# Kernel optimization log

Hardware: AMD Instinct MI355X
Metric: run time of the kernel (lower is better)

## Reference

```python
import jax, jax.numpy as jnp
import numpy as np

N_NODES = 10000
N_EDGES = 640000
D_FEAT = 128


def setup_inputs() -> dict:
    key = jax.random.key(0)
    k1, k2, k3, k4 = jax.random.split(key, 4)
    edge_feat = jax.random.normal(k1, (N_EDGES, D_FEAT), dtype=jnp.float32)
    node_feat = jax.random.normal(k2, (N_NODES, D_FEAT), dtype=jnp.float32)
    recv_idx = jax.random.randint(k3, (N_EDGES,), 0, N_NODES, dtype=jnp.int64 if jax.config.jax_enable_x64 else jnp.int32)
    W = jax.random.normal(k4, (2 * D_FEAT, D_FEAT), dtype=jnp.float32) * (1.0 / np.sqrt(2 * D_FEAT))
    b = jnp.zeros((D_FEAT,), dtype=jnp.float32)
    return {"edge_feat": edge_feat, "node_feat": node_feat, "recv_idx": recv_idx, "W": W, "b": b}


def reference(edge_feat, node_feat, recv_idx, W, b):
    # Unsorted segment sum: scatter-add edge features into receiver nodes. [E,d] -> [N,d]
    n_nodes = node_feat.shape[0]
    agg = jax.ops.segment_sum(edge_feat, recv_idx, num_segments=n_nodes)
    # Concat node features with aggregated received-edge features. [N, 2d]
    collected = jnp.concatenate([node_feat, agg], axis=-1)
    # node_model: Linear(2d -> d)
    return collected @ W + b
```

## Files before the change

### kernel.cpp

```cpp
#include <hip/hip_runtime.h>

#define N_NODES 10000
#define N_EDGES 640000
#define D_FEAT 128

#define HB   64
#define HBLK 1024
#define EPB  (N_EDGES / HB)
#define BCS  10016

#define WS_BCNT   0
#define WS_BSUM   641024
#define WS_START  641088
#define WS_SORTED 651392
#define WS_AGG    1291392

__global__ __launch_bounds__(HBLK) void hist_kernel(
        const int* __restrict__ recv, int* __restrict__ bcnt) {
    __shared__ int h[N_NODES];
    for (int i = threadIdx.x; i < N_NODES; i += HBLK) h[i] = 0;
    __syncthreads();
    const int4* r4 = (const int4*)(recv + blockIdx.x * EPB);
    for (int i = threadIdx.x; i < EPB / 4; i += HBLK) {
        const int4 r = r4[i];
        atomicAdd(&h[r.x], 1);
        atomicAdd(&h[r.y], 1);
        atomicAdd(&h[r.z], 1);
        atomicAdd(&h[r.w], 1);
    }
    __syncthreads();
    int* dst = bcnt + blockIdx.x * BCS;
    for (int i = threadIdx.x; i < N_NODES; i += HBLK) dst[i] = h[i];
}

__global__ __launch_bounds__(256) void scan1_kernel(
        int* __restrict__ bcnt, int* __restrict__ start, int* __restrict__ bsum) {
    __shared__ int s_w[4];
    const int tid = threadIdx.x;
    const int n   = blockIdx.x * 256 + tid;
    const bool ok = (n < N_NODES);

    int tot = 0;
    if (ok) {
        int run = 0;
        #pragma unroll
        for (int b = 0; b < HB; ++b) {
            int* p = bcnt + b * BCS + n;
            const int c = *p;
            *p = run;
            run += c;
        }
        tot = run;
    }
    const int lane = tid & 63;
    const int wave = tid >> 6;
    int x = tot;
    #pragma unroll
    for (int off = 1; off < 64; off <<= 1) {
        int t = __shfl_up(x, off, 64);
        if (lane >= off) x += t;
    }
    if (lane == 63) s_w[wave] = x;
    __syncthreads();
    int woff = 0;
    #pragma unroll
    for (int k = 0; k < 3; ++k) woff += (k < wave) ? s_w[k] : 0;
    if (ok) start[n] = woff + x - tot;
    if (tid == 0) bsum[blockIdx.x] = s_w[0] + s_w[1] + s_w[2] + s_w[3];
}

__global__ __launch_bounds__(256) void scan2_kernel(
        const int* __restrict__ bsum, int* __restrict__ start) {
    __shared__ int s_boff;
    const int tid = threadIdx.x;
    if (tid == 0) {
        int acc = 0;
        for (int k = 0; k < (int)blockIdx.x; ++k) acc += bsum[k];
        s_boff = acc;
        if (blockIdx.x == 0) start[N_NODES] = N_EDGES;
    }
    __syncthreads();
    const int n = blockIdx.x * 256 + tid;
    if (n < N_NODES) start[n] += s_boff;
}

__global__ __launch_bounds__(HBLK) void reorder_kernel(
        const int* __restrict__ recv, const int* __restrict__ bcnt,
        const int* __restrict__ start, int* __restrict__ sorted) {
    __shared__ int cur[N_NODES];
    const int* rel = bcnt + blockIdx.x * BCS;
    for (int i = threadIdx.x; i < N_NODES; i += HBLK)
        cur[i] = start[i] + rel[i];
    __syncthreads();
    const int ebase = blockIdx.x * EPB;
    const int4* r4 = (const int4*)(recv + ebase);
    for (int i = threadIdx.x; i < EPB / 4; i += HBLK) {
        const int4 r = r4[i];
        const int e = ebase + i * 4;
        sorted[atomicAdd(&cur[r.x], 1)] = e + 0;
        sorted[atomicAdd(&cur[r.y], 1)] = e + 1;
        sorted[atomicAdd(&cur[r.z], 1)] = e + 2;
        sorted[atomicAdd(&cur[r.w], 1)] = e + 3;
    }
}

#define GW 16
__global__ __launch_bounds__(512) void gather_kernel(
        const float4* __restrict__ edge_feat4,
        const int* __restrict__ sorted_eid,
        const int* __restrict__ start,
        float4* __restrict__ agg4) {
    __shared__ float4 red[GW][32];
    const int n   = blockIdx.x;
    const int tid = threadIdx.x;
    const int l   = tid & 31;
    const int w   = tid >> 5;
    const int s = start[n];
    const int e = start[n + 1];
    float4 acc = {0.f, 0.f, 0.f, 0.f};
    int i = s + w;
    if (i < e) {
        int eid = sorted_eid[i];
        while (true) {
            const int inext = i + GW;
            const int eid_next = (inext < e) ? sorted_eid[inext] : 0;
            const float4 v = edge_feat4[(long)eid * 32 + l];
            acc.x += v.x; acc.y += v.y; acc.z += v.z; acc.w += v.w;
            i = inext;
            if (i >= e) break;
            eid = eid_next;
        }
    }
    red[w][l] = acc;
    __syncthreads();
    if (w == 0) {
        float4 r = red[0][l];
        #pragma unroll
        for (int g = 1; g < GW; ++g) {
            const float4 t = red[g][l];
            r.x += t.x; r.y += t.y; r.z += t.z; r.w += t.w;
        }
        agg4[(long)n * 32 + l] = r;
    }
}

__global__ __launch_bounds__(256) void gemm_kernel(
        const float* __restrict__ node_feat,
        const float* __restrict__ agg,
        const float* __restrict__ W,
        const float* __restrict__ b,
        float* __restrict__ out) {
    __shared__ __align__(16) float As[32][68];
    __shared__ __align__(16) float Bs[32][64];
    const int tid = threadIdx.x;
    const int tx = tid & 15;
    const int ty = tid >> 4;
    const int m0 = blockIdx.x * 64;
    const int n0 = blockIdx.y * 64;

    float acc[4][4] = {};

    for (int kt = 0; kt < 2 * D_FEAT; kt += 32) {
        const float* src = (kt < D_FEAT) ? (node_feat + kt) : (agg + (kt - D_FEAT));
        {
            const int r  = tid >> 3;
            const int c4 = tid & 7;
            #pragma unroll
            for (int p = 0; p < 2; ++p) {
                int row = m0 + p * 32 + r;
                row = (row < N_NODES) ? row : (N_NODES - 1);
                const float4 a4 = *(const float4*)(src + (long)row * D_FEAT + c4 * 4);
                As[c4 * 4 + 0][p * 32 + r] = a4.x;
                As[c4 * 4 + 1][p * 32 + r] = a4.y;
                As[c4 * 4 + 2][p * 32 + r] = a4.z;
                As[c4 * 4 + 3][p * 32 + r] = a4.w;
            }
        }
        {
            const int r  = tid >> 4;
            const int c4 = tid & 15;
            #pragma unroll
            for (int p = 0; p < 2; ++p) {
                const int row = kt + p * 16 + r;
                *(float4*)&Bs[p * 16 + r][c4 * 4] =
                    *(const float4*)(W + (long)row * D_FEAT + n0 + c4 * 4);
            }
        }
        __syncthreads();
        #pragma unroll
        for (int kk = 0; kk < 32; ++kk) {
            const float4 a4 = *(const float4*)&As[kk][ty * 4];
            const float4 b4 = *(const float4*)&Bs[kk][tx * 4];
            acc[0][0] += a4.x * b4.x; acc[0][1] += a4.x * b4.y;
            acc[0][2] += a4.x * b4.z; acc[0][3] += a4.x * b4.w;
            acc[1][0] += a4.y * b4.x; acc[1][1] += a4.y * b4.y;
            acc[1][2] += a4.y * b4.z; acc[1][3] += a4.y * b4.w;
            acc[2][0] += a4.z * b4.x; acc[2][1] += a4.z * b4.y;
            acc[2][2] += a4.z * b4.z; acc[2][3] += a4.z * b4.w;
            acc[3][0] += a4.w * b4.x; acc[3][1] += a4.w * b4.y;
            acc[3][2] += a4.w * b4.z; acc[3][3] += a4.w * b4.w;
        }
        __syncthreads();
    }

    const float4 bias = *(const float4*)(b + n0 + tx * 4);
    #pragma unroll
    for (int i2 = 0; i2 < 4; ++i2) {
        const int row = m0 + ty * 4 + i2;
        if (row < N_NODES) {
            float4 o;
            o.x = acc[i2][0] + bias.x;
            o.y = acc[i2][1] + bias.y;
            o.z = acc[i2][2] + bias.z;
            o.w = acc[i2][3] + bias.w;
            *(float4*)(out + (long)row * D_FEAT + n0 + tx * 4) = o;
        }
    }
}

extern "C" void kernel_launch(void* const* d_in, const int* in_sizes, int n_in,
                              void* d_out, int out_size, void* d_ws, size_t ws_size,
                              hipStream_t stream) {
    const float* edge_feat = (const float*)d_in[0];
    const float* node_feat = (const float*)d_in[1];
    const int*   recv      = (const int*)d_in[2];
    const float* W         = (const float*)d_in[3];
    const float* b         = (const float*)d_in[4];
    float* out = (float*)d_out;

    int* wsi    = (int*)d_ws;
    int* bcnt   = wsi + WS_BCNT;
    int* bsum   = wsi + WS_BSUM;
    int* startp = wsi + WS_START;
    int* sorted = wsi + WS_SORTED;
    float* agg  = (float*)(wsi + WS_AGG);

    hist_kernel<<<HB, HBLK, 0, stream>>>(recv, bcnt);
    scan1_kernel<<<(N_NODES + 255) / 256, 256, 0, stream>>>(bcnt, startp, bsum);
    scan2_kernel<<<(N_NODES + 255) / 256, 256, 0, stream>>>(bsum, startp);
    reorder_kernel<<<HB, HBLK, 0, stream>>>(recv, bcnt, startp, sorted);
    gather_kernel<<<N_NODES, 512, 0, stream>>>(
        (const float4*)edge_feat, sorted, startp, (float4*)agg);
    dim3 ggrid((N_NODES + 63) / 64, D_FEAT / 64);
    gemm_kernel<<<ggrid, 256, 0, stream>>>(node_feat, agg, W, b, out);
}
```

Measured before the change: 488.0 us.

## Assign one wavefront per node in gather and double histogram block count

The gather kernel moves from one 512-thread block per node with a shared-memory reduction to one 64-lane wavefront per node. Each half-wave walks alternating edges with four loads in flight per step, and the two halves are combined with a shuffle, which removes the LDS reduction and __syncthreads. The histogram and reorder stages now run as 128 blocks of 512 threads instead of 64 of 1024, which spreads them over more CUs but doubles the per-block count buffer and the serial scan length. Each node now has less in-flight parallelism, so latency hiding depends on the unrolled loads.

```diff
diff --git a/kernel.cpp b/kernel.cpp
--- a/kernel.cpp
+++ b/kernel.cpp
@@ -4,16 +4,16 @@
 #define N_EDGES 640000
 #define D_FEAT 128
 
-#define HB   64
-#define HBLK 1024
+#define HB   128
+#define HBLK 512
 #define EPB  (N_EDGES / HB)
 #define BCS  10016
 
 #define WS_BCNT   0
-#define WS_BSUM   641024
-#define WS_START  641088
-#define WS_SORTED 651392
-#define WS_AGG    1291392
+#define WS_BSUM   1282048
+#define WS_START  1282112
+#define WS_SORTED 1292160
+#define WS_AGG    1932160
 
 __global__ __launch_bounds__(HBLK) void hist_kernel(
         const int* __restrict__ recv, int* __restrict__ bcnt) {
@@ -43,7 +43,7 @@
     int tot = 0;
     if (ok) {
         int run = 0;
-        #pragma unroll
+        #pragma unroll 16
         for (int b = 0; b < HB; ++b) {
             int* p = bcnt + b * BCS + n;
             const int c = *p;
@@ -104,44 +104,65 @@
     }
 }
 
-#define GW 16
-__global__ __launch_bounds__(512) void gather_kernel(
+__global__ __launch_bounds__(256) void gather_kernel(
         const float4* __restrict__ edge_feat4,
         const int* __restrict__ sorted_eid,
         const int* __restrict__ start,
         float4* __restrict__ agg4) {
-    __shared__ float4 red[GW][32];
-    const int n   = blockIdx.x;
-    const int tid = threadIdx.x;
-    const int l   = tid & 31;
-    const int w   = tid >> 5;
+    const int tid  = threadIdx.x;
+    const int n    = blockIdx.x * 4 + (tid >> 6);
+    const int lane = tid & 63;
+    const int half = lane >> 5;
+    const int l    = lane & 31;
+
     const int s = start[n];
     const int e = start[n + 1];
     float4 acc = {0.f, 0.f, 0.f, 0.f};
-    int i = s + w;
-    if (i < e) {
-        int eid = sorted_eid[i];
-        while (true) {
-            const int inext = i + GW;
-            const int eid_next = (inext < e) ? sorted_eid[inext] : 0;
-            const float4 v = edge_feat4[(long)eid * 32 + l];
-            acc.x += v.x; acc.y += v.y; acc.z += v.z; acc.w += v.w;
-            i = inext;
-            if (i >= e) break;
-            eid = eid_next;
-        }
-    }
-    red[w][l] = acc;
-    __syncthreads();
-    if (w == 0) {
-        float4 r = red[0][l];
-        #pragma unroll
-        for (int g = 1; g < GW; ++g) {
-            const float4 t = red[g][l];
-            r.x += t.x; r.y += t.y; r.z += t.z; r.w += t.w;
-        }
-        agg4[(long)n * 32 + l] = r;
-    }
+
+    int i = s + half;
+    if (i + 6 < e) {
+        int e0 = sorted_eid[i];
+        int e1 = sorted_eid[i + 2];
+        int e2 = sorted_eid[i + 4];
+        int e3 = sorted_eid[i + 6];
+        i += 8;
+        while (i + 6 < e) {
+            const int f0 = sorted_eid[i];
+            const int f1 = sorted_eid[i + 2];
+            const int f2 = sorted_eid[i + 4];
+            const int f3 = sorted_eid[i + 6];
+            const float4 v0 = edge_feat4[(long)e0 * 32 + l];
+            const float4 v1 = edge_feat4[(long)e1 * 32 + l];
+            const float4 v2 = edge_feat4[(long)e2 * 32 + l];
+            const float4 v3 = edge_feat4[(long)e3 * 32 + l];
+            acc.x += (v0.x + v1.x) + (v2.x + v3.x);
+            acc.y += (v0.y + v1.y) + (v2.y + v3.y);
+            acc.z += (v0.z + v1.z) + (v2.z + v3.z);
+            acc.w += (v0.w + v1.w) + (v2.w + v3.w);
+            e0 = f0; e1 = f1; e2 = f2; e3 = f3;
+            i += 8;
+        }
+        const float4 v0 = edge_feat4[(long)e0 * 32 + l];
+        const float4 v1 = edge_feat4[(long)e1 * 32 + l];
+        const float4 v2 = edge_feat4[(long)e2 * 32 + l];
+        const float4 v3 = edge_feat4[(long)e3 * 32 + l];
+        acc.x += (v0.x + v1.x) + (v2.x + v3.x);
+        acc.y += (v0.y + v1.y) + (v2.y + v3.y);
+        acc.z += (v0.z + v1.z) + (v2.z + v3.z);
+        acc.w += (v0.w + v1.w) + (v2.w + v3.w);
+    }
+    for (; i < e; i += 2) {
+        const float4 v = edge_feat4[(long)sorted_eid[i] * 32 + l];
+        acc.x += v.x; acc.y += v.y; acc.z += v.z; acc.w += v.w;
+    }
+
+    float4 o;
+    o.x = acc.x + __shfl(acc.x, lane + 32, 64);
+    o.y = acc.y + __shfl(acc.y, lane + 32, 64);
+    o.z = acc.z + __shfl(acc.z, lane + 32, 64);
+    o.w = acc.w + __shfl(acc.w, lane + 32, 64);
+    if (half == 0)
+        agg4[(long)n * 32 + l] = o;
 }
 
 __global__ __launch_bounds__(256) void gemm_kernel(
@@ -239,7 +260,7 @@
     scan1_kernel<<<(N_NODES + 255) / 256, 256, 0, stream>>>(bcnt, startp, bsum);
     scan2_kernel<<<(N_NODES + 255) / 256, 256, 0, stream>>>(bsum, startp);
     reorder_kernel<<<HB, HBLK, 0, stream>>>(recv, bcnt, startp, sorted);
-    gather_kernel<<<N_NODES, 512, 0, stream>>>(
+    gather_kernel<<<N_NODES / 4, 256, 0, stream>>>(
         (const float4*)edge_feat, sorted, startp, (float4*)agg);
     dim3 ggrid((N_NODES + 63) / 64, D_FEAT / 64);
     gemm_kernel<<<ggrid, 256, 0, stream>>>(node_feat, agg, W, b, out);
```

Result: no change. 488.3 us (+0.1%).
